# Kernel tuning notes

Measured on AMD Instinct MI355X. Metric: run time of the kernel, lower is better.

Reference implementation:

```python
import jax, jax.numpy as jnp
import numpy as np

N = 20000
E = 320000
C = 16   # in_channels
G = 8    # growth_channels
H = 16   # kernel MLP hidden = RDB in_channels
DIM = 3
OMEGA = 100.0
BETA = 0.2


def _u(k, shape, s):
    return jax.random.uniform(k, shape, jnp.float32, -s, s)


def setup_inputs() -> dict:
    key = jax.random.key(0)
    ks = jax.random.split(key, 64)
    x = jax.random.normal(ks[0], (N, C), jnp.float32)
    pos = jax.random.normal(ks[1], (N, DIM), jnp.float32)
    # random edges with no self loops (add_remaining_self_loops appends them in reference)
    src = jax.random.randint(ks[2], (E,), 0, N)
    off = jax.random.randint(ks[3], (E,), 1, N)
    dst = (src + off) % N
    edge_index = jnp.stack([src, dst])
    d = {"x": x, "edge_index": edge_index, "pos": pos}
    ins = [C, C + G, C + 2 * G]
    outs = [G, G, C]
    i = 4
    for ci, (cin, cout) in enumerate(zip(ins, outs), 1):
        # SineLayer weights: uniform(-1/in_features, 1/in_features); biases ~ torch Linear default
        d[f"c{ci}_w0"] = _u(ks[i], (H, DIM + 1), 1.0 / (DIM + 1)); i += 1
        d[f"c{ci}_b0"] = _u(ks[i], (H,), 1.0 / np.sqrt(DIM + 1)); i += 1
        d[f"c{ci}_w1"] = _u(ks[i], (H, H), 1.0 / H); i += 1
        d[f"c{ci}_b1"] = _u(ks[i], (H,), 1.0 / np.sqrt(H)); i += 1
        d[f"c{ci}_w2"] = _u(ks[i], (H, H), 1.0 / H); i += 1
        d[f"c{ci}_b2"] = _u(ks[i], (H,), 1.0 / np.sqrt(H)); i += 1
        # final Linear(hidden -> in_size), stored transposed as [in_size, hidden]
        d[f"c{ci}_wl"] = _u(ks[i], (cin, H), 1.0 / np.sqrt(H)); i += 1
        d[f"c{ci}_bl"] = _u(ks[i], (cin,), 1.0 / np.sqrt(H)); i += 1
        d[f"c{ci}_bias"] = jnp.zeros((1, cout), jnp.float32); i += 1
    return d


def _edge_feat(pos, src, dst):
    # rel_pos = pos[dst] - pos[src]; spherical (rho, theta/pi, phi/pi), NaN at rho=0 -> 0
    rel = pos[dst] - pos[src]                              # [E,3]
    sq = jnp.sum(rel * rel, axis=1)
    zero = sq <= 0.0                                       # self loops
    rho = jnp.where(zero, 0.0, jnp.sqrt(jnp.where(zero, 1.0, sq)))
    theta = jnp.arctan2(jnp.where(zero, 0.0, rel[:, 1]), jnp.where(zero, 1.0, rel[:, 0]))
    phi = jnp.arcsin(jnp.clip(jnp.where(zero, 0.0, rel[:, 2]) / jnp.where(zero, 1.0, rho), -1.0, 1.0))
    return jnp.stack([rho, theta / jnp.pi, phi / jnp.pi], axis=1)  # [E,3]


def _gconv(feat, x, src, dst, n, out_ch, w0, b0, w1, b1, w2, b2, wl, bl, bias):
    # vectorized over output channels: channel index c is the 4th input of sin0
    base = feat @ w0[:, :3].T + b0                          # [E,H]
    ch = jnp.arange(out_ch, dtype=feat.dtype)               # [O]
    h = jnp.sin(OMEGA * (base[:, None, :] + ch[None, :, None] * w0[:, 3]))   # [E,O,H]
    h = jnp.sin(OMEGA * (jnp.einsum('eoh,gh->eog', h, w1) + b1))
    h = jnp.sin(OMEGA * (jnp.einsum('eoh,gh->eog', h, w2) + b2))
    xj = x[src]                                             # [E,in]
    # msg[e,o] = (Wl h[e,o] + bl) . x_j[e]  ==  h[e,o] . (Wl^T x_j[e]) + bl . x_j[e]
    msg = jnp.einsum('eoh,eh->eo', h, xj @ wl) + (xj @ bl)[:, None]
    return jax.ops.segment_sum(msg, dst, num_segments=n) + bias


def reference(x, edge_index, pos,
              c1_w0, c1_b0, c1_w1, c1_b1, c1_w2, c1_b2, c1_wl, c1_bl, c1_bias,
              c2_w0, c2_b0, c2_w1, c2_b1, c2_w2, c2_b2, c2_wl, c2_bl, c2_bias,
              c3_w0, c3_b0, c3_w1, c3_b1, c3_w2, c3_b2, c3_wl, c3_bl, c3_bias):
    n = x.shape[0]
    loop = jnp.arange(n, dtype=edge_index.dtype)
    src = jnp.concatenate([edge_index[0], loop])
    dst = jnp.concatenate([edge_index[1], loop])
    feat = _edge_feat(pos, src, dst)
    x1 = jax.nn.selu(_gconv(feat, x, src, dst, n, G, c1_w0, c1_b0, c1_w1, c1_b1, c1_w2, c1_b2, c1_wl, c1_bl, c1_bias))
    x2 = jax.nn.selu(_gconv(feat, jnp.concatenate([x, x1], 1), src, dst, n, G, c2_w0, c2_b0, c2_w1, c2_b1, c2_w2, c2_b2, c2_wl, c2_bl, c2_bias))
    x3 = jax.nn.selu(_gconv(feat, jnp.concatenate([x, x1, x2], 1), src, dst, n, C, c3_w0, c3_b0, c3_w1, c3_b1, c3_w2, c3_b2, c3_wl, c3_bl, c3_bias))
    return x + BETA * x3
```

## Files before the change

### kernel.cpp

```cpp
#include <hip/hip_runtime.h>
#include <math.h>

#define N_NODES 20000
#define N_EDGES 320000
#define HID 16
#define OMEGA 100.0f
#define BETA 0.2f
#define REVC 0.15915494309189535f

#define OFF_W0I 0
#define OFF_B1  64
#define OFF_B2  80
#define OFF_A2  128
#define OFF_AO  896
#define OFF_H2V 9088
#define P_SIZE  9472

typedef float  f32x4 __attribute__((ext_vector_type(4)));
typedef short  s16x8 __attribute__((ext_vector_type(8)));

__device__ __forceinline__ float sinrev(float x) { return __builtin_amdgcn_sinf(x); }
__device__ __forceinline__ float cosrev(float x) { return __builtin_amdgcn_cosf(x); }
__device__ __forceinline__ float fract_f(float x) { return __builtin_amdgcn_fractf(x); }

__device__ __forceinline__ float selu_f(float v) {
    const float a  = 1.6732632423543772f;
    const float sc = 1.0507009873554805f;
    return sc * (v > 0.f ? v : a * expm1f(v));
}

__device__ __forceinline__ f32x4 mfma16(s16x8 a, s16x8 b, f32x4 c) {
    return __builtin_amdgcn_mfma_f32_16x16x32_bf16(a, b, c, 0, 0, 0);
}

__device__ __forceinline__ unsigned pk_hi(float a, float b) {
    return (__float_as_uint(b) & 0xFFFF0000u) | (__float_as_uint(a) >> 16);
}
__device__ __forceinline__ float lo_of(float a) {
    return a - __uint_as_float(__float_as_uint(a) & 0xFFFF0000u);
}

union U4 { uint4 v; s16x8 s; };

struct PrepArgs {
    const float* w0[3]; const float* b0[3]; const float* w1[3]; const float* b1[3];
    const float* w2[3]; const float* b2[3];
    float* P[3];
};

__global__ __launch_bounds__(256) void prep_kernel(PrepArgs A)
{
    const int OUTS[3] = {8, 8, 16};
    int c = blockIdx.x;
    int OUT = OUTS[c];
    const float* w0 = A.w0[c]; const float* b0 = A.b0[c];
    const float* w1 = A.w1[c]; const float* b1 = A.b1[c];
    const float* w2 = A.w2[c]; const float* b2 = A.b2[c];
    float* P = A.P[c];
    unsigned* Pu = (unsigned*)P;

    __shared__ float W1s[256], W2s[256], cosB[256], sinB[256], w0c[16];
    int t = threadIdx.x;
    const float s = OMEGA * REVC;
    W1s[t] = s * w1[t];
    W2s[t] = s * w2[t];
    if (t < 16) w0c[t] = s * w0[t * 4 + 3];
    __syncthreads();

    if (t < 64) { int h = t >> 2, k = t & 3; P[t] = (k < 3) ? s * w0[h * 4 + k] : s * b0[h]; }
    if (t >= 64 && t < 80)  P[t] = s * b1[t - 64];
    if (t >= 80 && t < 96)  P[t] = s * b2[t - 80];

    if (t < OUT * 16) {
        int o = t >> 4, h = t & 15;
        float ang = fract_f((float)o * w0c[h]);
        cosB[t] = cosrev(ang);
        sinB[t] = sinrev(ang);
    }
    __syncthreads();

    if (t < 64) {
        int g = t & 15, q = t >> 4;
        float w[4], l[4];
#pragma unroll
        for (int j = 0; j < 4; j++) { w[j] = W2s[g * 16 + 4 * q + j]; l[j] = lo_of(w[j]); }
        ((uint4*)(Pu + OFF_A2))[t] = make_uint4(pk_hi(w[0], w[1]), pk_hi(w[2], w[3]),
                                                pk_hi(l[0], l[1]), pk_hi(l[2], l[3]));
    }
    for (int idx = t; idx < OUT * 64; idx += 256) {
        int o = idx >> 6, lane = idx & 63, g = lane & 15, q = lane >> 4;
        float v[8], l[8];
#pragma unroll
        for (int e = 0; e < 8; e++) {
            int k = 8 * q + e;
            float a = (k < 16) ? W1s[g * 16 + k] * cosB[o * 16 + k]
                               : W1s[g * 16 + (k - 16)] * sinB[o * 16 + (k - 16)];
            v[e] = a; l[e] = lo_of(a);
        }
        ((uint4*)(Pu + OFF_AO + o * 512))[lane] =
            make_uint4(pk_hi(v[0], v[1]), pk_hi(v[2], v[3]), pk_hi(v[4], v[5]), pk_hi(v[6], v[7]));
        ((uint4*)(Pu + OFF_AO + o * 512 + 256))[lane] =
            make_uint4(pk_hi(l[0], l[1]), pk_hi(l[2], l[3]), pk_hi(l[4], l[5]), pk_hi(l[6], l[7]));
    }
    if (t < OUT) {
        float oc = (float)t;
        float h0[HID], h1[HID];
#pragma unroll
        for (int h = 0; h < HID; h++)
            h0[h] = sinrev(fract_f(fmaf(oc, w0c[h], s * b0[h])));
#pragma unroll
        for (int g = 0; g < HID; g++) {
            float sa = s * b1[g];
#pragma unroll
            for (int h = 0; h < HID; h++) sa += h0[h] * W1s[g * HID + h];
            h1[g] = sinrev(sa);
        }
#pragma unroll
        for (int g = 0; g < HID; g++) {
            float sa = s * b2[g];
#pragma unroll
            for (int h = 0; h < HID; h++) sa += h1[h] * W2s[g * HID + h];
            P[OFF_H2V + t * HID + g] = sinrev(sa);
        }
    }
}

__global__ __launch_bounds__(256) void fused_pre_kernel(
    const int* __restrict__ ei, const float* __restrict__ pos,
    const float* __restrict__ x,
    float4* __restrict__ feat, float* __restrict__ xcat,
    const float* __restrict__ wl1, const float* __restrict__ bl1,
    float* __restrict__ tb, float* __restrict__ blxb)
{
    int b = blockIdx.x;
    if (b < 1250) {
        int e = b * 256 + threadIdx.x;
        if (e >= N_EDGES) return;
        int s = ei[e], d = ei[N_EDGES + e];
        float rx = pos[d * 3 + 0] - pos[s * 3 + 0];
        float ry = pos[d * 3 + 1] - pos[s * 3 + 1];
        float rz = pos[d * 3 + 2] - pos[s * 3 + 2];
        float sq = rx * rx + ry * ry + rz * rz;
        float4 f = make_float4(0.f, 0.f, 0.f, 0.f);
        if (sq > 0.f) {
            float rho = sqrtf(sq);
            float th  = atan2f(ry, rx);
            float ph  = asinf(fminf(fmaxf(rz / rho, -1.f), 1.f));
            const float inv_pi = 0.31830988618379067f;
            f = make_float4(rho, th * inv_pi, ph * inv_pi, 0.f);
        }
        feat[e] = f;
    } else if (b < 2500) {
        int i = (b - 1250) * 256 + threadIdx.x;
        if (i >= N_NODES * 16) return;
        int n = i >> 4, cc = i & 15;
        xcat[n * 32 + cc] = x[i];
    } else {
        int n = (b - 2500) * 256 + threadIdx.x;
        if (n >= N_NODES) return;
        float tn[HID];
#pragma unroll
        for (int h = 0; h < HID; h++) tn[h] = 0.f;
        float bx = 0.f;
#pragma unroll
        for (int i = 0; i < 16; i++) {
            float xi = x[n * 16 + i];
            bx += bl1[i] * xi;
#pragma unroll
            for (int h = 0; h < HID; h++) tn[h] += wl1[i * 16 + h] * xi;
        }
#pragma unroll
        for (int h = 0; h < HID; h++) tb[n * 16 + h] = tn[h];
        blxb[n] = bx;
    }
}

template<int OUT>
__global__ __launch_bounds__(256) void conv_kernel(
    const int* __restrict__ ei, const float4* __restrict__ feat,
    const float* __restrict__ tbn, const float* __restrict__ blxn,
    const float* __restrict__ P, float* __restrict__ acc)
{
    constexpr int L2O = (OUT == 16) ? 4 : 3;
    constexpr int EPI = 64 / OUT;
    constexpr int NI  = 16 / EPI;

    __shared__ float sm[4][OUT * 4 * 17];
    const unsigned* Pu = (const unsigned*)P;
    int wslot = threadIdx.x >> 6;
    int wid  = (blockIdx.x * 256 + threadIdx.x) >> 6;
    int lane = threadIdx.x & 63;
    int e16 = lane & 15, q = lane >> 4;
    int e = wid * 16 + e16;
    int src = ei[e];
    int dst = ei[N_EDGES + e];
    float4 f = feat[e];

    f32x4 T = *(const f32x4*)(tbn + src * 16 + 4 * q);
    float bx = blxn[src];

    float tr[8];
    {
        const float4* w0i = (const float4*)P;
        int hb = (q & 1) * 8;
#pragma unroll
        for (int j = 0; j < 8; j++) {
            float4 w = w0i[hb + j];
            float ang = fract_f(w.w + f.x * w.x + f.y * w.y + f.z * w.z);
            tr[j] = (q < 2) ? sinrev(ang) : cosrev(ang);
        }
    }
    U4 Bh, Bl;
    Bh.v = make_uint4(pk_hi(tr[0], tr[1]), pk_hi(tr[2], tr[3]),
                      pk_hi(tr[4], tr[5]), pk_hi(tr[6], tr[7]));
    Bl.v = make_uint4(pk_hi(lo_of(tr[0]), lo_of(tr[1])), pk_hi(lo_of(tr[2]), lo_of(tr[3])),
                      pk_hi(lo_of(tr[4]), lo_of(tr[5])), pk_hi(lo_of(tr[6]), lo_of(tr[7])));

    U4 A2; A2.v = ((const uint4*)(Pu + OFF_A2))[lane];
    f32x4 c1 = *(const f32x4*)(P + OFF_B1 + 4 * q);
    f32x4 c2 = *(const f32x4*)(P + OFF_B2 + 4 * q);

#pragma unroll 2
    for (int o = 0; o < OUT; ++o) {
        U4 Ah, Al;
        Ah.v = ((const uint4*)(Pu + OFF_AO + o * 512))[lane];
        Al.v = ((const uint4*)(Pu + OFF_AO + o * 512 + 256))[lane];
        f32x4 D = c1;
        D = mfma16(Ah.s, Bh.s, D);
        D = mfma16(Ah.s, Bl.s, D);
        D = mfma16(Al.s, Bh.s, D);
        float h1[4];
#pragma unroll
        for (int j = 0; j < 4; j++) h1[j] = sinrev(D[j]);
        unsigned p0 = pk_hi(h1[0], h1[1]), p1 = pk_hi(h1[2], h1[3]);
        unsigned l0 = pk_hi(lo_of(h1[0]), lo_of(h1[1])), l1 = pk_hi(lo_of(h1[2]), lo_of(h1[3]));
        U4 Ph, Pl;
        Ph.v = make_uint4(p0, p1, p0, p1);
        Pl.v = make_uint4(l0, l1, l0, l1);
        f32x4 D2 = c2;
        D2 = mfma16(A2.s, Ph.s, D2);
        D2 = mfma16(A2.s, Pl.s, D2);
        float p = sinrev(D2[0]) * T[0] + sinrev(D2[1]) * T[1]
                + sinrev(D2[2]) * T[2] + sinrev(D2[3]) * T[3];
        if (q == 0) p += bx;
        sm[wslot][(o * 4 + q) * 17 + e16] = p;
    }

    int oo = lane & (OUT - 1);
    int el = lane >> L2O;
#pragma unroll
    for (int j = 0; j < NI; j++) {
        int ej = j * EPI + el;
        int dj = __shfl(dst, ej);
        float v = sm[wslot][(oo * 4 + 0) * 17 + ej] + sm[wslot][(oo * 4 + 1) * 17 + ej]
                + sm[wslot][(oo * 4 + 2) * 17 + ej] + sm[wslot][(oo * 4 + 3) * 17 + ej];
        atomicAdd(&acc[dj * OUT + oo], v);
    }
}

template<int OUT, int CO>
__global__ __launch_bounds__(256) void finish_mid_kernel(
    const float* __restrict__ acc, const float* __restrict__ bias,
    const float* __restrict__ h2v,
    float* __restrict__ tb, float* __restrict__ blxb,
    float* __restrict__ xcat,
    const float* __restrict__ wlN, const float* __restrict__ blN)
{
    int n = blockIdx.x * 256 + threadIdx.x;
    if (n >= N_NODES) return;
    float trr[HID];
#pragma unroll
    for (int h = 0; h < HID; h++) trr[h] = tb[n * 16 + h];
    float bx = blxb[n];
    float xrow[CO + OUT];
#pragma unroll
    for (int i = 0; i < CO; i++) xrow[i] = xcat[n * 32 + i];
#pragma unroll
    for (int o = 0; o < OUT; o++) {
        float m = bx;
#pragma unroll
        for (int h = 0; h < HID; h++) m += h2v[o * 16 + h] * trr[h];
        float v = selu_f(acc[n * OUT + o] + bias[o] + m);
        xrow[CO + o] = v;
        xcat[n * 32 + CO + o] = v;
    }
    float tn[HID];
#pragma unroll
    for (int h = 0; h < HID; h++) tn[h] = 0.f;
    float bxn = 0.f;
#pragma unroll
    for (int i = 0; i < CO + OUT; i++) {
        float xi = xrow[i];
        bxn += blN[i] * xi;
#pragma unroll
        for (int h = 0; h < HID; h++) tn[h] += wlN[i * 16 + h] * xi;
    }
#pragma unroll
    for (int h = 0; h < HID; h++) tb[n * 16 + h] = tn[h];
    blxb[n] = bxn;
}

__global__ __launch_bounds__(256) void finish_out_kernel(
    const float* __restrict__ acc, const float* __restrict__ bias,
    const float* __restrict__ h2v,
    const float* __restrict__ tb, const float* __restrict__ blxb,
    const float* __restrict__ x, float* __restrict__ out)
{
    int n = blockIdx.x * 256 + threadIdx.x;
    if (n >= N_NODES) return;
    float trr[HID];
#pragma unroll
    for (int h = 0; h < HID; h++) trr[h] = tb[n * 16 + h];
    float bx = blxb[n];
#pragma unroll
    for (int c = 0; c < 16; c++) {
        float m = bx;
#pragma unroll
        for (int h = 0; h < HID; h++) m += h2v[c * 16 + h] * trr[h];
        out[n * 16 + c] = x[n * 16 + c] + BETA * selu_f(acc[n * 16 + c] + bias[c] + m);
    }
}

extern "C" void kernel_launch(void* const* d_in, const int* in_sizes, int n_in,
                              void* d_out, int out_size, void* d_ws, size_t ws_size,
                              hipStream_t stream)
{
    const float* x   = (const float*)d_in[0];
    const int*   ei  = (const int*)d_in[1];
    const float* pos = (const float*)d_in[2];

    const float* W[27];
    for (int i = 0; i < 27; i++) W[i] = (const float*)d_in[3 + i];

    float* ws    = (float*)d_ws;
    float4* feat = (float4*)ws;
    float* xcat  = ws + (size_t)N_EDGES * 4;
    float* acc1  = xcat + (size_t)N_NODES * 32;
    float* acc2  = acc1 + (size_t)N_NODES * 8;
    float* acc3  = acc2 + (size_t)N_NODES * 8;
    float* P1    = acc3 + (size_t)N_NODES * 16;
    float* P2    = P1 + P_SIZE;
    float* P3    = P2 + P_SIZE;
    float* tb    = P3 + P_SIZE;
    float* blxb  = tb + (size_t)N_NODES * 16;
    float* out   = (float*)d_out;

    hipMemsetAsync(acc1, 0, (size_t)N_NODES * 32 * sizeof(float), stream);

    PrepArgs pa;
    for (int c = 0; c < 3; c++) {
        pa.w0[c] = W[9 * c + 0]; pa.b0[c] = W[9 * c + 1];
        pa.w1[c] = W[9 * c + 2]; pa.b1[c] = W[9 * c + 3];
        pa.w2[c] = W[9 * c + 4]; pa.b2[c] = W[9 * c + 5];
    }
    pa.P[0] = P1; pa.P[1] = P2; pa.P[2] = P3;

    dim3 blk(256);
    prep_kernel<<<3, blk, 0, stream>>>(pa);
    fused_pre_kernel<<<2579, blk, 0, stream>>>(ei, pos, x, feat, xcat, W[6], W[7], tb, blxb);

    conv_kernel<8><<<5000, blk, 0, stream>>>(ei, feat, tb, blxb, P1, acc1);
    finish_mid_kernel<8, 16><<<79, blk, 0, stream>>>(acc1, W[8], P1 + OFF_H2V, tb, blxb, xcat, W[15], W[16]);

    conv_kernel<8><<<5000, blk, 0, stream>>>(ei, feat, tb, blxb, P2, acc2);
    finish_mid_kernel<8, 24><<<79, blk, 0, stream>>>(acc2, W[17], P2 + OFF_H2V, tb, blxb, xcat, W[24], W[25]);

    conv_kernel<16><<<5000, blk, 0, stream>>>(ei, feat, tb, blxb, P3, acc3);
    finish_out_kernel<<<79, blk, 0, stream>>>(acc3, W[26], P3 + OFF_H2V, tb, blxb, x, out);
}
```

Baseline: 167.5 us.

## Sort edges by destination via counting sort before the conv kernels

Adds a histogram, single-block scan and atomic scatter that reorder the edges by destination node, writing sorted src, dst and edge features. The three conv kernels then read the sorted arrays, so consecutive edges mostly share a destination. This is meant to make the atomic accumulation into acc more local and less contended. It adds three extra launches, including a serial one-block scan, plus extra workspace traffic. The order of equal-destination edges is nondeterministic, so floating-point sums can vary slightly between runs.

```diff
diff --git a/kernel.cpp b/kernel.cpp
--- a/kernel.cpp
+++ b/kernel.cpp
@@ -8,7 +8,6 @@
 #define BETA 0.2f
 #define REVC 0.15915494309189535f
 
-#define OFF_W0I 0
 #define OFF_B1  64
 #define OFF_B2  80
 #define OFF_A2  128
@@ -125,38 +124,73 @@
     }
 }
 
-__global__ __launch_bounds__(256) void fused_pre_kernel(
+__global__ __launch_bounds__(256) void hist_kernel(
+    const int* __restrict__ ei, int* __restrict__ cnt)
+{
+    int e = blockIdx.x * 256 + threadIdx.x;
+    if (e >= N_EDGES) return;
+    atomicAdd(&cnt[ei[N_EDGES + e]], 1);
+}
+
+__global__ __launch_bounds__(256) void scan_kernel(
+    const int* __restrict__ cnt, int* __restrict__ cursor)
+{
+    __shared__ int tot[256], excl[256];
+    int t = threadIdx.x;
+    int base = t * 79;
+    int end  = min(base + 79, N_NODES);
+    int s = 0;
+    for (int i = base; i < end; i++) s += cnt[i];
+    tot[t] = s;
+    __syncthreads();
+    if (t == 0) {
+        int run = 0;
+        for (int i = 0; i < 256; i++) { excl[i] = run; run += tot[i]; }
+    }
+    __syncthreads();
+    int run = excl[t];
+    for (int i = base; i < end; i++) { cursor[i] = run; run += cnt[i]; }
+}
+
+__global__ __launch_bounds__(256) void scatter_kernel(
     const int* __restrict__ ei, const float* __restrict__ pos,
-    const float* __restrict__ x,
-    float4* __restrict__ feat, float* __restrict__ xcat,
+    int* __restrict__ cursor,
+    int* __restrict__ ssrc, int* __restrict__ sdst, float4* __restrict__ sfeat)
+{
+    int e = blockIdx.x * 256 + threadIdx.x;
+    if (e >= N_EDGES) return;
+    int s = ei[e], d = ei[N_EDGES + e];
+    int p = atomicAdd(&cursor[d], 1);
+    ssrc[p] = s;
+    sdst[p] = d;
+    float rx = pos[d * 3 + 0] - pos[s * 3 + 0];
+    float ry = pos[d * 3 + 1] - pos[s * 3 + 1];
+    float rz = pos[d * 3 + 2] - pos[s * 3 + 2];
+    float sq = rx * rx + ry * ry + rz * rz;
+    float4 f = make_float4(0.f, 0.f, 0.f, 0.f);
+    if (sq > 0.f) {
+        float rho = sqrtf(sq);
+        float th  = atan2f(ry, rx);
+        float ph  = asinf(fminf(fmaxf(rz / rho, -1.f), 1.f));
+        const float inv_pi = 0.31830988618379067f;
+        f = make_float4(rho, th * inv_pi, ph * inv_pi, 0.f);
+    }
+    sfeat[p] = f;
+}
+
+__global__ __launch_bounds__(256) void pre_kernel(
+    const float* __restrict__ x, float* __restrict__ xcat,
     const float* __restrict__ wl1, const float* __restrict__ bl1,
     float* __restrict__ tb, float* __restrict__ blxb)
 {
     int b = blockIdx.x;
     if (b < 1250) {
-        int e = b * 256 + threadIdx.x;
-        if (e >= N_EDGES) return;
-        int s = ei[e], d = ei[N_EDGES + e];
-        float rx = pos[d * 3 + 0] - pos[s * 3 + 0];
-        float ry = pos[d * 3 + 1] - pos[s * 3 + 1];
-        float rz = pos[d * 3 + 2] - pos[s * 3 + 2];
-        float sq = rx * rx + ry * ry + rz * rz;
-        float4 f = make_float4(0.f, 0.f, 0.f, 0.f);
-        if (sq > 0.f) {
-            float rho = sqrtf(sq);
-            float th  = atan2f(ry, rx);
-            float ph  = asinf(fminf(fmaxf(rz / rho, -1.f), 1.f));
-            const float inv_pi = 0.31830988618379067f;
-            f = make_float4(rho, th * inv_pi, ph * inv_pi, 0.f);
-        }
-        feat[e] = f;
-    } else if (b < 2500) {
-        int i = (b - 1250) * 256 + threadIdx.x;
+        int i = b * 256 + threadIdx.x;
         if (i >= N_NODES * 16) return;
         int n = i >> 4, cc = i & 15;
         xcat[n * 32 + cc] = x[i];
     } else {
-        int n = (b - 2500) * 256 + threadIdx.x;
+        int n = (b - 1250) * 256 + threadIdx.x;
         if (n >= N_NODES) return;
         float tn[HID];
 #pragma unroll
@@ -177,7 +211,8 @@
 
 template<int OUT>
 __global__ __launch_bounds__(256) void conv_kernel(
-    const int* __restrict__ ei, const float4* __restrict__ feat,
+    const int* __restrict__ ssrc, const int* __restrict__ sdst,
+    const float4* __restrict__ sfeat,
     const float* __restrict__ tbn, const float* __restrict__ blxn,
     const float* __restrict__ P, float* __restrict__ acc)
 {
@@ -192,9 +227,9 @@
     int lane = threadIdx.x & 63;
     int e16 = lane & 15, q = lane >> 4;
     int e = wid * 16 + e16;
-    int src = ei[e];
-    int dst = ei[N_EDGES + e];
-    float4 f = feat[e];
+    int src = ssrc[e];
+    int dst = sdst[e];
+    float4 f = sfeat[e];
 
     f32x4 T = *(const f32x4*)(tbn + src * 16 + 4 * q);
     float bx = blxn[src];
@@ -333,7 +368,7 @@
     for (int i = 0; i < 27; i++) W[i] = (const float*)d_in[3 + i];
 
     float* ws    = (float*)d_ws;
-    float4* feat = (float4*)ws;
+    float4* sfeat = (float4*)ws;
     float* xcat  = ws + (size_t)N_EDGES * 4;
     float* acc1  = xcat + (size_t)N_NODES * 32;
     float* acc2  = acc1 + (size_t)N_NODES * 8;
@@ -343,9 +378,14 @@
     float* P3    = P2 + P_SIZE;
     float* tb    = P3 + P_SIZE;
     float* blxb  = tb + (size_t)N_NODES * 16;
+    int*   ssrc  = (int*)(blxb + N_NODES);
+    int*   sdst  = ssrc + N_EDGES;
+    int*   cnt   = sdst + N_EDGES;
+    int*   cursor= cnt + N_NODES;
     float* out   = (float*)d_out;
 
     hipMemsetAsync(acc1, 0, (size_t)N_NODES * 32 * sizeof(float), stream);
+    hipMemsetAsync(cnt, 0, (size_t)N_NODES * sizeof(int), stream);
 
     PrepArgs pa;
     for (int c = 0; c < 3; c++) {
@@ -356,15 +396,20 @@
     pa.P[0] = P1; pa.P[1] = P2; pa.P[2] = P3;
 
     dim3 blk(256);
+    dim3 ge((N_EDGES + 255) / 256);
+
     prep_kernel<<<3, blk, 0, stream>>>(pa);
-    fused_pre_kernel<<<2579, blk, 0, stream>>>(ei, pos, x, feat, xcat, W[6], W[7], tb, blxb);
-
-    conv_kernel<8><<<5000, blk, 0, stream>>>(ei, feat, tb, blxb, P1, acc1);
+    hist_kernel<<<ge, blk, 0, stream>>>(ei, cnt);
+    scan_kernel<<<1, blk, 0, stream>>>(cnt, cursor);
+    scatter_kernel<<<ge, blk, 0, stream>>>(ei, pos, cursor, ssrc, sdst, sfeat);
+    pre_kernel<<<1329, blk, 0, stream>>>(x, xcat, W[6], W[7], tb, blxb);
+
+    conv_kernel<8><<<5000, blk, 0, stream>>>(ssrc, sdst, sfeat, tb, blxb, P1, acc1);
     finish_mid_kernel<8, 16><<<79, blk, 0, stream>>>(acc1, W[8], P1 + OFF_H2V, tb, blxb, xcat, W[15], W[16]);
 
-    conv_kernel<8><<<5000, blk, 0, stream>>>(ei, feat, tb, blxb, P2, acc2);
+    conv_kernel<8><<<5000, blk, 0, stream>>>(ssrc, sdst, sfeat, tb, blxb, P2, acc2);
     finish_mid_kernel<8, 24><<<79, blk, 0, stream>>>(acc2, W[17], P2 + OFF_H2V, tb, blxb, xcat, W[24], W[25]);
 
-    conv_kernel<16><<<5000, blk, 0, stream>>>(ei, feat, tb, blxb, P3, acc3);
+    conv_kernel<16><<<5000, blk, 0, stream>>>(ssrc, sdst, sfeat, tb, blxb, P3, acc3);
     finish_out_kernel<<<79, blk, 0, stream>>>(acc3, W[26], P3 + OFF_H2V, tb, blxb, x, out);
 }
```

Result: slower. 288.3 us (+72.1%).
